# Optimization experiments

Measured on AMD Instinct MI355X. Metric: run time of the kernel, lower is better.

## Reference

```python
import jax, jax.numpy as jnp
import numpy as np
import math

D_MODEL = 1024
N_HEADS = 16
HEAD_DIM = D_MODEL // N_HEADS
B, T = 4, 2048


def setup_inputs() -> dict:
    key = jax.random.key(0)
    k1, k2, k3, k4, k5 = jax.random.split(key, 5)
    s = 1.0 / math.sqrt(D_MODEL)
    return {
        "x": jax.random.normal(k1, (B, T, D_MODEL), dtype=jnp.float32),
        "qkv_w": jax.random.normal(k2, (3 * D_MODEL, D_MODEL), dtype=jnp.float32) * s,
        "qkv_b": jax.random.normal(k3, (3 * D_MODEL,), dtype=jnp.float32) * 0.02,
        "out_w": jax.random.normal(k4, (D_MODEL, D_MODEL), dtype=jnp.float32) * s,
        "out_b": jax.random.normal(k5, (D_MODEL,), dtype=jnp.float32) * 0.02,
    }


def reference(x, qkv_w, qkv_b, out_w, out_b) -> jnp.ndarray:
    b, t, c = x.shape
    h, hd = N_HEADS, HEAD_DIM
    # qkv projection: [B,T,3C]
    qkv = jnp.einsum("btc,oc->bto", x, qkv_w) + qkv_b
    qkv = qkv.reshape(b, t, 3, h, hd).transpose(2, 0, 3, 1, 4)  # [3,B,H,T,hd]
    q, k, v = qkv[0], qkv[1], qkv[2]
    scale = 1.0 / math.sqrt(hd)
    attn = jnp.einsum("bhqd,bhkd->bhqk", q, k) * scale  # [B,H,T,T]
    causal = jnp.triu(jnp.ones((t, t), dtype=bool), k=1)
    attn = jnp.where(causal, -jnp.inf, attn)
    attn = jax.nn.softmax(attn, axis=-1)
    out = jnp.einsum("bhqk,bhkd->bhqd", attn, v)  # [B,H,T,hd]
    out = out.transpose(0, 2, 1, 3).reshape(b, t, c)
    return jnp.einsum("btc,oc->bto", out, out_w) + out_b
```

## Files before the change

kernel.cpp:

```cpp
#include <hip/hip_runtime.h>
#include <stdint.h>
#include <stddef.h>

#define TT 2048
#define NH 16
#define HD 64
#define CM 1024
#define QSCALE 0.1803368801f
#define PPAD 72

typedef float f32x4  __attribute__((ext_vector_type(4)));
typedef short bf16x8 __attribute__((ext_vector_type(8)));

static __device__ __forceinline__ unsigned short f32_to_bf16(float f) {
    union { float f; unsigned u; } c; c.f = f;
    unsigned u = c.u;
    u += 0x7FFFu + ((u >> 16) & 1u);
    return (unsigned short)(u >> 16);
}

static __device__ __forceinline__ unsigned pack_bf16_trunc(float lo, float hi) {
    return __builtin_amdgcn_perm(__float_as_uint(hi), __float_as_uint(lo), 0x07060302u);
}

static __device__ __forceinline__ void glds16(const unsigned short* g, unsigned short* l) {
    __builtin_amdgcn_global_load_lds(
        (const __attribute__((address_space(1))) unsigned int*)g,
        (__attribute__((address_space(3))) unsigned int*)l,
        16, 0, 0);
}

static __device__ __forceinline__ void hard_barrier() {
    asm volatile("s_waitcnt vmcnt(0) lgkmcnt(0)" ::: "memory");
    __syncthreads();
}

__global__ __launch_bounds__(256) void cast_all(
    const float* __restrict__ x, const float* __restrict__ w1,
    const float* __restrict__ w2,
    unsigned short* __restrict__ X16, unsigned short* __restrict__ W1o,
    unsigned short* __restrict__ W2o) {
    int i = blockIdx.x * blockDim.x + threadIdx.x;
    const float* src; unsigned short* dst; int j;
    if (i < 2097152)      { src = x;  dst = X16; j = i; }
    else if (i < 2883584) { src = w1; dst = W1o; j = i - 2097152; }
    else                  { src = w2; dst = W2o; j = i - 2883584; }
    float4 v = ((const float4*)src)[j];
    ushort4 o;
    o.x = f32_to_bf16(v.x); o.y = f32_to_bf16(v.y);
    o.z = f32_to_bf16(v.z); o.w = f32_to_bf16(v.w);
    ((ushort4*)dst)[j] = o;
}

template<bool SWAP>
__device__ __forceinline__ void gemm256_core(
    const unsigned short* __restrict__ A,
    const unsigned short* __restrict__ Bm,
    int m0, int n0,
    unsigned short* lds,
    f32x4 acc[8][4])
{
    const int tid  = threadIdx.x;
    const int lane = tid & 63;
    const int w    = tid >> 6;
    const int l15  = lane & 15;
    const int quad = lane >> 4;
    const int wm   = (w >> 1) * 128;
    const int wn   = (w & 1) * 64;
    const int ro   = (quad ^ (l15 & 3)) * 8;

    const int rr = tid >> 2;
    const int ch = (tid & 3) ^ (rr & 3);
    const unsigned short* gA = A  + (size_t)(m0 + rr) * CM + ch * 8;
    const unsigned short* gB = Bm + (size_t)(n0 + rr) * CM + ch * 8;
    const int wb = (tid & ~63) * 8;

    unsigned short* ldsA = lds;
    unsigned short* ldsB = lds + 16384;

#define STAGE6(bb)                                                    \
    {                                                                 \
        unsigned short* dA = ldsA + (bb) * 8192 + wb;                 \
        unsigned short* dB = ldsB + (bb) * 4096 + wb;                 \
        glds16(gA,            dA);                                    \
        glds16(gA +  64 * CM, dA + 2048);                             \
        glds16(gA + 128 * CM, dA + 4096);                             \
        glds16(gA + 192 * CM, dA + 6144);                             \
        glds16(gB,            dB);                                    \
        glds16(gB +  64 * CM, dB + 2048);                             \
        gA += 32; gB += 32;                                           \
    }

    STAGE6(0);
    STAGE6(1);

    for (int t = 0; t < 32; ++t) {
        if (t > 0) {
            asm volatile("s_waitcnt lgkmcnt(0)" ::: "memory");
            __builtin_amdgcn_s_barrier();
            asm volatile("" ::: "memory");
            if (t + 1 < 32) STAGE6((t + 1) & 1);
        }
        if (t + 1 < 32) asm volatile("s_waitcnt vmcnt(6)" ::: "memory");
        else            asm volatile("s_waitcnt vmcnt(0)" ::: "memory");
        __builtin_amdgcn_s_barrier();
        asm volatile("" ::: "memory");

        const unsigned short* tA = ldsA + (t & 1) * 8192;
        const unsigned short* tB = ldsB + (t & 1) * 4096;

        bf16x8 bfr[4];
        #pragma unroll
        for (int ni = 0; ni < 4; ++ni)
            bfr[ni] = *(const bf16x8*)(tB + (wn + ni * 16 + l15) * 32 + ro);
        bf16x8 af[8];
        #pragma unroll
        for (int mi = 0; mi < 8; ++mi)
            af[mi] = *(const bf16x8*)(tA + (wm + mi * 16 + l15) * 32 + ro);

        #pragma unroll
        for (int mi = 0; mi < 8; ++mi)
            #pragma unroll
            for (int ni = 0; ni < 4; ++ni)
                acc[mi][ni] = SWAP
                    ? __builtin_amdgcn_mfma_f32_16x16x32_bf16(bfr[ni], af[mi], acc[mi][ni], 0, 0, 0)
                    : __builtin_amdgcn_mfma_f32_16x16x32_bf16(af[mi], bfr[ni], acc[mi][ni], 0, 0, 0);
    }
#undef STAGE6
}

__global__ __launch_bounds__(256, 2) void gemm_qkv(
    const unsigned short* __restrict__ X,
    const unsigned short* __restrict__ W,
    const float* __restrict__ bias,
    unsigned short* __restrict__ Qb,
    unsigned short* __restrict__ Kb,
    unsigned short* __restrict__ Vt)
{
    __shared__ __align__(16) unsigned short lds[24576];
    const int m0 = blockIdx.y * 256;
    const int n0 = blockIdx.x * 128;

    f32x4 acc[8][4];
    f32x4 z = {0.f, 0.f, 0.f, 0.f};
    #pragma unroll
    for (int mi = 0; mi < 8; ++mi)
        #pragma unroll
        for (int ni = 0; ni < 4; ++ni) acc[mi][ni] = z;

    const int region = n0 >> 10;
    if (region < 2) gemm256_core<true >(X, W, m0, n0, lds, acc);
    else            gemm256_core<false>(X, W, m0, n0, lds, acc);

    const int tid  = threadIdx.x;
    const int lane = tid & 63;
    const int w    = tid >> 6;
    const int wm   = (w >> 1) * 128;
    const int wn   = (w & 1) * 64;
    const int l15  = lane & 15;
    const int quad = lane >> 4;
    const int b_idx = m0 >> 11;
    const int t0 = m0 & 2047;

    if (region == 2) {
        hard_barrier();
        #pragma unroll
        for (int hn = 0; hn < 2; ++hn) {
            if ((w & 1) == hn) {
                #pragma unroll
                for (int ni = 0; ni < 4; ++ni) {
                    const int nloc = ni * 16 + l15;
                    const float bv = bias[n0 + hn * 64 + nloc];
                    #pragma unroll
                    for (int mi = 0; mi < 8; ++mi) {
                        uint2 pk;
                        pk.x = (unsigned)f32_to_bf16(acc[mi][ni][0] + bv) |
                               ((unsigned)f32_to_bf16(acc[mi][ni][1] + bv) << 16);
                        pk.y = (unsigned)f32_to_bf16(acc[mi][ni][2] + bv) |
                               ((unsigned)f32_to_bf16(acc[mi][ni][3] + bv) << 16);
                        *(uint2*)(lds + nloc * 264 + wm + mi * 16 + quad * 4) = pk;
                    }
                }
            }
            hard_barrier();
            {
                const int row = tid >> 2, seg = tid & 3;
                const int o   = n0 + hn * 64 + row;
                const int oin = o & 1023;
                const int hh  = oin >> 6, d = oin & 63;
                unsigned short* dst = Vt + ((size_t)((b_idx << 4) + hh) * HD + d) * TT
                                        + t0 + seg * 64;
                const unsigned short* src = lds + row * 264 + seg * 64;
                #pragma unroll
                for (int u = 0; u < 8; ++u)
                    *(uint4*)(dst + u * 8) = *(const uint4*)(src + u * 8);
            }
            hard_barrier();
        }
        return;
    }

    unsigned short* dst0 = region ? Kb : Qb;
    const float scl = region ? 1.0f : QSCALE;
    #pragma unroll
    for (int mi = 0; mi < 8; ++mi) {
        const int gm = m0 + wm + mi * 16 + l15;
        const int t  = gm & 2047;
        #pragma unroll
        for (int ni = 0; ni < 4; ++ni) {
            const int o  = n0 + wn + ni * 16 + quad * 4;
            const float4 bv = *(const float4*)(bias + o);
            const int oin = o & 1023;
            const int hh = oin >> 6, d = oin & 63;
            const int bh = (b_idx << 4) + hh;
            const float v0 = (acc[mi][ni][0] + bv.x) * scl;
            const float v1 = (acc[mi][ni][1] + bv.y) * scl;
            const float v2 = (acc[mi][ni][2] + bv.z) * scl;
            const float v3 = (acc[mi][ni][3] + bv.w) * scl;
            uint2 pk;
            pk.x = (unsigned)f32_to_bf16(v0) | ((unsigned)f32_to_bf16(v1) << 16);
            pk.y = (unsigned)f32_to_bf16(v2) | ((unsigned)f32_to_bf16(v3) << 16);
            *(uint2*)(dst0 + (((size_t)(bh * TT + t)) << 6) + d) = pk;
        }
    }
}

__global__ __launch_bounds__(256, 2) void attn_kernel(
    const unsigned short* __restrict__ Qb,
    const unsigned short* __restrict__ Kb,
    const unsigned short* __restrict__ Vt,
    unsigned short* __restrict__ CTX)
{
    __shared__ __align__(16) unsigned short Kl[2][64 * 64];
    __shared__ __align__(16) unsigned short Vl[2][64 * 64];
    __shared__ __align__(16) unsigned short Pl[8][16 * PPAD];

    const int id = blockIdx.x;
    const int qt = 15 - (id >> 6);
    const int bh = id & 63;
    const int b  = bh >> 4, h = bh & 15;
    const int tid  = threadIdx.x;
    const int lane = tid & 63;
    const int w    = tid >> 6;
    const int l15  = lane & 15;
    const int quad = lane >> 4;
    const int sw   = l15 & 7;
    const int bhh  = b * NH + h;

    const unsigned short* Kbase = Kb + (size_t)bhh * TT * HD;
    const unsigned short* Vbase = Vt + (size_t)bhh * HD * TT;
    const f32x4 z = {0.f, 0.f, 0.f, 0.f};

    const int c1 = tid, c2 = tid + 256;
    const int row1 = c1 >> 3, col1 = ((c1 & 7) ^ (row1 & 7)) * 8;
    const int row2 = c2 >> 3, col2 = ((c2 & 7) ^ (row2 & 7)) * 8;
    unsigned short* dK1 = &Kl[0][(c1 & ~63) * 8];
    unsigned short* dK2 = &Kl[0][(c2 & ~63) * 8];
    unsigned short* dV1 = &Vl[0][(c1 & ~63) * 8];
    unsigned short* dV2 = &Vl[0][(c2 & ~63) * 8];

    const int kt_last = 2 * qt + 1;
    const int qb0 = qt * 128;

    const unsigned short* kp1 = Kbase + (size_t)row1 * HD + col1;
    const unsigned short* kp2 = Kbase + (size_t)row2 * HD + col2;
    const unsigned short* vp1 = Vbase + (size_t)row1 * TT + col1;
    const unsigned short* vp2 = Vbase + (size_t)row2 * TT + col2;

    bf16x8 qf[2][2];
    #pragma unroll
    for (int f = 0; f < 2; ++f) {
        const unsigned short* qr =
            Qb + (size_t)(bhh * TT + qb0 + f * 64 + w * 16 + l15) * HD + quad * 8;
        qf[f][0] = *(const bf16x8*)(qr);
        qf[f][1] = *(const bf16x8*)(qr + 32);
    }

    f32x4 o_acc[2][4];
    #pragma unroll
    for (int f = 0; f < 2; ++f)
        #pragma unroll
        for (int di = 0; di < 4; ++di) o_acc[f][di] = z;
    float lrun[2] = {0.f, 0.f};

    glds16(kp1, dK1); glds16(kp2, dK2);
    glds16(vp1, dV1); glds16(vp2, dV2);
    kp1 += 64 * HD; kp2 += 64 * HD; vp1 += 64; vp2 += 64;

    for (int kt = 0; kt <= kt_last; ++kt) {
        const int cur = kt & 1;
        hard_barrier();
        if (kt < kt_last) {
            const int nx = (cur ^ 1) * 4096;
            glds16(kp1, dK1 + nx); glds16(kp2, dK2 + nx);
            glds16(vp1, dV1 + nx); glds16(vp2, dV2 + nx);
            kp1 += 64 * HD; kp2 += 64 * HD; vp1 += 64; vp2 += 64;
        }

        const unsigned short* Kt = Kl[cur];
        const unsigned short* Vtile = Vl[cur];
        const bool f0act = (kt < kt_last);

        f32x4 s0[4], s1[4];
        #pragma unroll
        for (int ni = 0; ni < 4; ++ni) {
            const unsigned short* kr = Kt + (ni * 16 + l15) * 64;
            bf16x8 kf0 = *(const bf16x8*)(kr + ((quad ^ sw) * 8));
            bf16x8 kf1 = *(const bf16x8*)(kr + (((quad + 4) ^ sw) * 8));
            if (f0act) {
                f32x4 a = __builtin_amdgcn_mfma_f32_16x16x32_bf16(kf0, qf[0][0], z, 0, 0, 0);
                s0[ni] = __builtin_amdgcn_mfma_f32_16x16x32_bf16(kf1, qf[0][1], a, 0, 0, 0);
            }
            f32x4 a1 = __builtin_amdgcn_mfma_f32_16x16x32_bf16(kf0, qf[1][0], z, 0, 0, 0);
            s1[ni] = __builtin_amdgcn_mfma_f32_16x16x32_bf16(kf1, qf[1][1], a1, 0, 0, 0);
        }

        const int qloc = w * 16 + l15;
        if (f0act && kt == 2 * qt) {
            #pragma unroll
            for (int ni = 0; ni < 4; ++ni)
                #pragma unroll
                for (int r = 0; r < 4; ++r)
                    if (ni * 16 + quad * 4 + r > qloc) s0[ni][r] = -1e30f;
        }
        if (kt == kt_last) {
            #pragma unroll
            for (int ni = 0; ni < 4; ++ni)
                #pragma unroll
                for (int r = 0; r < 4; ++r)
                    if (ni * 16 + quad * 4 + r > qloc) s1[ni][r] = -1e30f;
        }

        #define SOFTMAX_P(S, F)                                              \
        {                                                                    \
            float acc_l = 0.f;                                               \
            _Pragma("unroll")                                                \
            for (int ni = 0; ni < 4; ++ni)                                   \
                _Pragma("unroll")                                            \
                for (int r = 0; r < 4; ++r) {                                \
                    float p = __builtin_amdgcn_exp2f(S[ni][r]);              \
                    S[ni][r] = p;                                            \
                    acc_l += p;                                              \
                }                                                            \
            lrun[F] += acc_l;                                                \
            unsigned short* pwf = Pl[w * 2 + F];                             \
            _Pragma("unroll")                                                \
            for (int ni = 0; ni < 4; ++ni) {                                 \
                uint2 pk;                                                    \
                pk.x = pack_bf16_trunc(S[ni][0], S[ni][1]);                  \
                pk.y = pack_bf16_trunc(S[ni][2], S[ni][3]);                  \
                *(uint2*)(pwf + l15 * PPAD + ni * 16 + quad * 4) = pk;       \
            }                                                                \
        }

        if (f0act) SOFTMAX_P(s0, 0);
        SOFTMAX_P(s1, 1);
        #undef SOFTMAX_P

        asm volatile("s_waitcnt lgkmcnt(0)" ::: "memory");

        const unsigned short* pw0 = Pl[w * 2 + 0];
        const unsigned short* pw1 = Pl[w * 2 + 1];
        if (f0act) {
            #pragma unroll
            for (int c = 0; c < 2; ++c) {
                bf16x8 pf0 = *(const bf16x8*)(pw0 + l15 * PPAD + c * 32 + quad * 8);
                bf16x8 pf1 = *(const bf16x8*)(pw1 + l15 * PPAD + c * 32 + quad * 8);
                #pragma unroll
                for (int di = 0; di < 4; ++di) {
                    const unsigned short* vr = Vtile + (di * 16 + l15) * 64
                                             + (((c * 4 + quad) ^ sw) * 8);
                    bf16x8 vf = *(const bf16x8*)(vr);
                    o_acc[0][di] = __builtin_amdgcn_mfma_f32_16x16x32_bf16(vf, pf0, o_acc[0][di], 0, 0, 0);
                    o_acc[1][di] = __builtin_amdgcn_mfma_f32_16x16x32_bf16(vf, pf1, o_acc[1][di], 0, 0, 0);
                }
            }
        } else {
            #pragma unroll
            for (int c = 0; c < 2; ++c) {
                bf16x8 pf1 = *(const bf16x8*)(pw1 + l15 * PPAD + c * 32 + quad * 8);
                #pragma unroll
                for (int di = 0; di < 4; ++di) {
                    const unsigned short* vr = Vtile + (di * 16 + l15) * 64
                                             + (((c * 4 + quad) ^ sw) * 8);
                    bf16x8 vf = *(const bf16x8*)(vr);
                    o_acc[1][di] = __builtin_amdgcn_mfma_f32_16x16x32_bf16(vf, pf1, o_acc[1][di], 0, 0, 0);
                }
            }
        }
    }

    #pragma unroll
    for (int f = 0; f < 2; ++f) {
        float lt = lrun[f];
        lt += __shfl_xor(lt, 16);
        lt += __shfl_xor(lt, 32);
        const float inv = 1.0f / lt;
        unsigned short* crow =
            CTX + (size_t)(b * TT + qb0 + f * 64 + w * 16 + l15) * CM + h * HD;
        #pragma unroll
        for (int di = 0; di < 4; ++di) {
            uint2 pk;
            pk.x = (unsigned)f32_to_bf16(o_acc[f][di][0] * inv) |
                   ((unsigned)f32_to_bf16(o_acc[f][di][1] * inv) << 16);
            pk.y = (unsigned)f32_to_bf16(o_acc[f][di][2] * inv) |
                   ((unsigned)f32_to_bf16(o_acc[f][di][3] * inv) << 16);
            *(uint2*)(crow + di * 16 + quad * 4) = pk;
        }
    }
}

__global__ __launch_bounds__(256, 2) void gemm_out(
    const unsigned short* __restrict__ CTX,
    const unsigned short* __restrict__ W,
    const float* __restrict__ bias,
    float* __restrict__ out)
{
    __shared__ __align__(16) unsigned short lds[24576];
    const int m0 = blockIdx.y * 256;
    const int n0 = blockIdx.x * 128;

    f32x4 acc[8][4];
    f32x4 z = {0.f, 0.f, 0.f, 0.f};
    #pragma unroll
    for (int mi = 0; mi < 8; ++mi)
        #pragma unroll
        for (int ni = 0; ni < 4; ++ni) acc[mi][ni] = z;

    gemm256_core<true>(CTX, W, m0, n0, lds, acc);

    const int tid  = threadIdx.x;
    const int lane = tid & 63;
    const int w    = tid >> 6;
    const int wm   = (w >> 1) * 128;
    const int wn   = (w & 1) * 64;
    const int l15  = lane & 15;
    const int quad = lane >> 4;

    #pragma unroll
    for (int mi = 0; mi < 8; ++mi) {
        const int gm = m0 + wm + mi * 16 + l15;
        float* orow = out + (size_t)gm * CM;
        #pragma unroll
        for (int ni = 0; ni < 4; ++ni) {
            const int o = n0 + wn + ni * 16 + quad * 4;
            const float4 bv = *(const float4*)(bias + o);
            float4 v;
            v.x = acc[mi][ni][0] + bv.x;
            v.y = acc[mi][ni][1] + bv.y;
            v.z = acc[mi][ni][2] + bv.z;
            v.w = acc[mi][ni][3] + bv.w;
            *(float4*)(orow + o) = v;
        }
    }
}

extern "C" void kernel_launch(void* const* d_in, const int* in_sizes, int n_in,
                              void* d_out, int out_size, void* d_ws, size_t ws_size,
                              hipStream_t stream) {
    const float* x     = (const float*)d_in[0];
    const float* qkv_w = (const float*)d_in[1];
    const float* qkv_b = (const float*)d_in[2];
    const float* out_w = (const float*)d_in[3];
    const float* out_b = (const float*)d_in[4];
    float* out = (float*)d_out;

    char* ws = (char*)d_ws;
    unsigned short* X16 = (unsigned short*)(ws + 0);
    unsigned short* W1  = (unsigned short*)(ws + 16777216);
    unsigned short* W2  = (unsigned short*)(ws + 23068672);
    unsigned short* Qb  = (unsigned short*)(ws + 25165824);
    unsigned short* Kb  = (unsigned short*)(ws + 41943040);
    unsigned short* Vt  = (unsigned short*)(ws + 58720256);
    unsigned short* CTX = (unsigned short*)(ws + 75497472);

    cast_all<<<12288, 256, 0, stream>>>(x, qkv_w, out_w, X16, W1, W2);

    gemm_qkv<<<dim3(24, 32), 256, 0, stream>>>(X16, W1, qkv_b, Qb, Kb, Vt);
    attn_kernel<<<1024, 256, 0, stream>>>(Qb, Kb, Vt, CTX);
    gemm_out<<<dim3(8, 32), 256, 0, stream>>>(CTX, W2, out_b, out);
}
```

Measured before the change: 256.1 us.

## Split long causal attention query tiles into two KV chunks with combine kernel

Query tiles 8-15 now have their key range split into two halves, each handled by its own block. The blocks write unnormalized bf16 partial outputs and row sums into reused workspace, and a new combine kernel merges them. Shorter tiles are interleaved so that no block does more than 16 key tiles, which balances per-block work across 1536 blocks. The cost is an extra kernel launch, extra partial-output traffic, and an extra bf16 rounding of the partials. The softmax row-sum reduction is also reassociated into a tree.

Result: slower. 271.1 us (+5.9%).

```diff
diff --git a/kernel.cpp b/kernel.cpp
--- a/kernel.cpp
+++ b/kernel.cpp
@@ -17,6 +17,10 @@
     unsigned u = c.u;
     u += 0x7FFFu + ((u >> 16) & 1u);
     return (unsigned short)(u >> 16);
+}
+
+static __device__ __forceinline__ float bf16_to_f32(unsigned short h) {
+    union { unsigned u; float f; } c; c.u = ((unsigned)h) << 16; return c.f;
 }
 
 static __device__ __forceinline__ unsigned pack_bf16_trunc(float lo, float hi) {
@@ -229,15 +233,27 @@
     const unsigned short* __restrict__ Qb,
     const unsigned short* __restrict__ Kb,
     const unsigned short* __restrict__ Vt,
-    unsigned short* __restrict__ CTX)
+    unsigned short* __restrict__ CTX,
+    unsigned short* __restrict__ PO,
+    float* __restrict__ PL)
 {
     __shared__ __align__(16) unsigned short Kl[2][64 * 64];
     __shared__ __align__(16) unsigned short Vl[2][64 * 64];
     __shared__ __align__(16) unsigned short Pl[8][16 * PPAD];
 
+    static const signed char E_QT[24]  = {15,15,14,13,12,11,10,9,8,7,14,6,13,5,12,4,11,3,10,2,9,1,8,0};
+    static const signed char E_C0[24]  = {0,16,0,0,0,0,0,0,0,0,16,0,16,0,16,0,16,0,16,0,16,0,16,0};
+    static const signed char E_LEN[24] = {16,16,16,16,16,16,16,16,16,16,14,14,12,12,10,10,8,8,6,6,4,4,2,2};
+    static const signed char E_SL[24]  = {14,15,12,10,8,6,4,2,0,-1,13,-1,11,-1,9,-1,7,-1,5,-1,3,-1,1,-1};
+
     const int id = blockIdx.x;
-    const int qt = 15 - (id >> 6);
+    const int e  = id >> 6;
     const int bh = id & 63;
+    const int qt   = E_QT[e];
+    const int c0   = E_C0[e];
+    const int len  = E_LEN[e];
+    const int slot = E_SL[e];
+
     const int b  = bh >> 4, h = bh & 15;
     const int tid  = threadIdx.x;
     const int lane = tid & 63;
@@ -259,13 +275,12 @@
     unsigned short* dV1 = &Vl[0][(c1 & ~63) * 8];
     unsigned short* dV2 = &Vl[0][(c2 & ~63) * 8];
 
-    const int kt_last = 2 * qt + 1;
     const int qb0 = qt * 128;
 
-    const unsigned short* kp1 = Kbase + (size_t)row1 * HD + col1;
-    const unsigned short* kp2 = Kbase + (size_t)row2 * HD + col2;
-    const unsigned short* vp1 = Vbase + (size_t)row1 * TT + col1;
-    const unsigned short* vp2 = Vbase + (size_t)row2 * TT + col2;
+    const unsigned short* kp1 = Kbase + (size_t)(c0 * 64 + row1) * HD + col1;
+    const unsigned short* kp2 = Kbase + (size_t)(c0 * 64 + row2) * HD + col2;
+    const unsigned short* vp1 = Vbase + (size_t)row1 * TT + c0 * 64 + col1;
+    const unsigned short* vp2 = Vbase + (size_t)row2 * TT + c0 * 64 + col2;
 
     bf16x8 qf[2][2];
     #pragma unroll
@@ -287,10 +302,11 @@
     glds16(vp1, dV1); glds16(vp2, dV2);
     kp1 += 64 * HD; kp2 += 64 * HD; vp1 += 64; vp2 += 64;
 
-    for (int kt = 0; kt <= kt_last; ++kt) {
-        const int cur = kt & 1;
+    for (int i = 0; i < len; ++i) {
+        const int kt  = c0 + i;
+        const int cur = i & 1;
         hard_barrier();
-        if (kt < kt_last) {
+        if (i + 1 < len) {
             const int nx = (cur ^ 1) * 4096;
             glds16(kp1, dK1 + nx); glds16(kp2, dK2 + nx);
             glds16(vp1, dV1 + nx); glds16(vp2, dV2 + nx);
@@ -299,7 +315,7 @@
 
         const unsigned short* Kt = Kl[cur];
         const unsigned short* Vtile = Vl[cur];
-        const bool f0act = (kt < kt_last);
+        const bool f0act = (kt < 2 * qt + 1);
 
         f32x4 s0[4], s1[4];
         #pragma unroll
@@ -323,7 +339,7 @@
                 for (int r = 0; r < 4; ++r)
                     if (ni * 16 + quad * 4 + r > qloc) s0[ni][r] = -1e30f;
         }
-        if (kt == kt_last) {
+        if (kt == 2 * qt + 1) {
             #pragma unroll
             for (int ni = 0; ni < 4; ++ni)
                 #pragma unroll
@@ -333,16 +349,17 @@
 
         #define SOFTMAX_P(S, F)                                              \
         {                                                                    \
-            float acc_l = 0.f;                                               \
+            float tni[4];                                                    \
             _Pragma("unroll")                                                \
-            for (int ni = 0; ni < 4; ++ni)                                   \
-                _Pragma("unroll")                                            \
-                for (int r = 0; r < 4; ++r) {                                \
-                    float p = __builtin_amdgcn_exp2f(S[ni][r]);              \
-                    S[ni][r] = p;                                            \
-                    acc_l += p;                                              \
-                }                                                            \
-            lrun[F] += acc_l;                                                \
+            for (int ni = 0; ni < 4; ++ni) {                                 \
+                float p0 = __builtin_amdgcn_exp2f(S[ni][0]);                 \
+                float p1 = __builtin_amdgcn_exp2f(S[ni][1]);                 \
+                float p2 = __builtin_amdgcn_exp2f(S[ni][2]);                 \
+                float p3 = __builtin_amdgcn_exp2f(S[ni][3]);                 \
+                S[ni][0] = p0; S[ni][1] = p1; S[ni][2] = p2; S[ni][3] = p3;  \
+                tni[ni] = (p0 + p1) + (p2 + p3);                             \
+            }                                                                \
+            lrun[F] += (tni[0] + tni[1]) + (tni[2] + tni[3]);                \
             unsigned short* pwf = Pl[w * 2 + F];                             \
             _Pragma("unroll")                                                \
             for (int ni = 0; ni < 4; ++ni) {                                 \
@@ -390,23 +407,86 @@
         }
     }
 
-    #pragma unroll
-    for (int f = 0; f < 2; ++f) {
-        float lt = lrun[f];
-        lt += __shfl_xor(lt, 16);
-        lt += __shfl_xor(lt, 32);
-        const float inv = 1.0f / lt;
-        unsigned short* crow =
-            CTX + (size_t)(b * TT + qb0 + f * 64 + w * 16 + l15) * CM + h * HD;
-        #pragma unroll
-        for (int di = 0; di < 4; ++di) {
-            uint2 pk;
-            pk.x = (unsigned)f32_to_bf16(o_acc[f][di][0] * inv) |
-                   ((unsigned)f32_to_bf16(o_acc[f][di][1] * inv) << 16);
-            pk.y = (unsigned)f32_to_bf16(o_acc[f][di][2] * inv) |
-                   ((unsigned)f32_to_bf16(o_acc[f][di][3] * inv) << 16);
-            *(uint2*)(crow + di * 16 + quad * 4) = pk;
-        }
+    if (slot < 0) {
+        #pragma unroll
+        for (int f = 0; f < 2; ++f) {
+            float lt = lrun[f];
+            lt += __shfl_xor(lt, 16);
+            lt += __shfl_xor(lt, 32);
+            const float inv = 1.0f / lt;
+            unsigned short* crow =
+                CTX + (size_t)(b * TT + qb0 + f * 64 + w * 16 + l15) * CM + h * HD;
+            #pragma unroll
+            for (int di = 0; di < 4; ++di) {
+                uint2 pk;
+                pk.x = (unsigned)f32_to_bf16(o_acc[f][di][0] * inv) |
+                       ((unsigned)f32_to_bf16(o_acc[f][di][1] * inv) << 16);
+                pk.y = (unsigned)f32_to_bf16(o_acc[f][di][2] * inv) |
+                       ((unsigned)f32_to_bf16(o_acc[f][di][3] * inv) << 16);
+                *(uint2*)(crow + di * 16 + quad * 4) = pk;
+            }
+        }
+    } else {
+        const size_t pb = ((size_t)slot * 64 + bh) * 8192;
+        const size_t lb = ((size_t)slot * 64 + bh) * 128;
+        #pragma unroll
+        for (int f = 0; f < 2; ++f) {
+            float lt = lrun[f];
+            lt += __shfl_xor(lt, 16);
+            lt += __shfl_xor(lt, 32);
+            const int row = f * 64 + w * 16 + l15;
+            if (quad == 0) PL[lb + row] = lt;
+            unsigned short* prow = PO + pb + (size_t)row * 64;
+            #pragma unroll
+            for (int di = 0; di < 4; ++di) {
+                uint2 pk;
+                pk.x = (unsigned)f32_to_bf16(o_acc[f][di][0]) |
+                       ((unsigned)f32_to_bf16(o_acc[f][di][1]) << 16);
+                pk.y = (unsigned)f32_to_bf16(o_acc[f][di][2]) |
+                       ((unsigned)f32_to_bf16(o_acc[f][di][3]) << 16);
+                *(uint2*)(prow + di * 16 + quad * 4) = pk;
+            }
+        }
+    }
+}
+
+__global__ __launch_bounds__(256) void attn_combine(
+    const unsigned short* __restrict__ PO,
+    const float* __restrict__ PL,
+    unsigned short* __restrict__ CTX)
+{
+    const int id = blockIdx.x;
+    const int qi = id >> 6;
+    const int bh = id & 63;
+    const int b = bh >> 4, h = bh & 15;
+    const size_t bA = ((size_t)(qi * 2 + 0) * 64 + bh) * 8192;
+    const size_t bB = ((size_t)(qi * 2 + 1) * 64 + bh) * 8192;
+    const size_t lA = ((size_t)(qi * 2 + 0) * 64 + bh) * 128;
+    const size_t lB = ((size_t)(qi * 2 + 1) * 64 + bh) * 128;
+    const int t = threadIdx.x;
+    #pragma unroll
+    for (int u = 0; u < 4; ++u) {
+        const int idx = u * 256 + t;
+        const int row = idx >> 3, d0 = (idx & 7) * 8;
+        const bf16x8 a = *(const bf16x8*)(PO + bA + row * 64 + d0);
+        const bf16x8 c = *(const bf16x8*)(PO + bB + row * 64 + d0);
+        const float inv = 1.0f / (PL[lA + row] + PL[lB + row]);
+        uint2 pk0, pk1;
+        float o0 = (bf16_to_f32((unsigned short)a[0]) + bf16_to_f32((unsigned short)c[0])) * inv;
+        float o1 = (bf16_to_f32((unsigned short)a[1]) + bf16_to_f32((unsigned short)c[1])) * inv;
+        float o2 = (bf16_to_f32((unsigned short)a[2]) + bf16_to_f32((unsigned short)c[2])) * inv;
+        float o3 = (bf16_to_f32((unsigned short)a[3]) + bf16_to_f32((unsigned short)c[3])) * inv;
+        float o4 = (bf16_to_f32((unsigned short)a[4]) + bf16_to_f32((unsigned short)c[4])) * inv;
+        float o5 = (bf16_to_f32((unsigned short)a[5]) + bf16_to_f32((unsigned short)c[5])) * inv;
+        float o6 = (bf16_to_f32((unsigned short)a[6]) + bf16_to_f32((unsigned short)c[6])) * inv;
+        float o7 = (bf16_to_f32((unsigned short)a[7]) + bf16_to_f32((unsigned short)c[7])) * inv;
+        pk0.x = (unsigned)f32_to_bf16(o0) | ((unsigned)f32_to_bf16(o1) << 16);
+        pk0.y = (unsigned)f32_to_bf16(o2) | ((unsigned)f32_to_bf16(o3) << 16);
+        pk1.x = (unsigned)f32_to_bf16(o4) | ((unsigned)f32_to_bf16(o5) << 16);
+        pk1.y = (unsigned)f32_to_bf16(o6) | ((unsigned)f32_to_bf16(o7) << 16);
+        unsigned short* dst = CTX + ((size_t)(b * TT + (8 + qi) * 128 + row)) * CM + h * HD + d0;
+        uint4 pk; pk.x = pk0.x; pk.y = pk0.y; pk.z = pk1.x; pk.w = pk1.y;
+        *(uint4*)dst = pk;
     }
 }
 
@@ -474,9 +554,13 @@
     unsigned short* Vt  = (unsigned short*)(ws + 58720256);
     unsigned short* CTX = (unsigned short*)(ws + 75497472);
 
+    unsigned short* PO = X16;
+    float*          PL = (float*)W1;
+
     cast_all<<<12288, 256, 0, stream>>>(x, qkv_w, out_w, X16, W1, W2);
 
     gemm_qkv<<<dim3(24, 32), 256, 0, stream>>>(X16, W1, qkv_b, Qb, Kb, Vt);
-    attn_kernel<<<1024, 256, 0, stream>>>(Qb, Kb, Vt, CTX);
+    attn_kernel<<<1536, 256, 0, stream>>>(Qb, Kb, Vt, CTX, PO, PL);
+    attn_combine<<<512, 256, 0, stream>>>(PO, PL, CTX);
     gemm_out<<<dim3(8, 32), 256, 0, stream>>>(CTX, W2, out_b, out);
 }
```

## Triple-buffer K/V tiles with explicit vmcnt waits and share one P buffer

Applied to the files above, without the earlier changes.

Moves the attention inner loop from double to triple buffering of K/V tiles in LDS, issuing loads two tiles ahead and using vmcnt-based waits plus barriers instead of a hard barrier. The P scratch buffer is cut from two per wave to one, so the s1 and s0 softmax/PV phases run one after the other, with V fragments cached in registers for reuse. This aims to hide global load latency and keep LDS usage roughly flat. The cost is extra barriers, higher register pressure from the held V fragments, and serialized P writes.

Result: slower. 262.0 us (+2.3%).

```diff
diff --git a/kernel.cpp b/kernel.cpp
--- a/kernel.cpp
+++ b/kernel.cpp
@@ -231,9 +231,9 @@
     const unsigned short* __restrict__ Vt,
     unsigned short* __restrict__ CTX)
 {
-    __shared__ __align__(16) unsigned short Kl[2][64 * 64];
-    __shared__ __align__(16) unsigned short Vl[2][64 * 64];
-    __shared__ __align__(16) unsigned short Pl[8][16 * PPAD];
+    __shared__ __align__(16) unsigned short Kl[3][4096];
+    __shared__ __align__(16) unsigned short Vl[3][4096];
+    __shared__ __align__(16) unsigned short Pl[4][16 * PPAD];
 
     const int id = blockIdx.x;
     const int qt = 15 - (id >> 6);
@@ -259,7 +259,7 @@
     unsigned short* dV1 = &Vl[0][(c1 & ~63) * 8];
     unsigned short* dV2 = &Vl[0][(c2 & ~63) * 8];
 
-    const int kt_last = 2 * qt + 1;
+    const int len = 2 * qt + 2;
     const int qb0 = qt * 128;
 
     const unsigned short* kp1 = Kbase + (size_t)row1 * HD + col1;
@@ -283,23 +283,34 @@
         for (int di = 0; di < 4; ++di) o_acc[f][di] = z;
     float lrun[2] = {0.f, 0.f};
 
-    glds16(kp1, dK1); glds16(kp2, dK2);
-    glds16(vp1, dV1); glds16(vp2, dV2);
-    kp1 += 64 * HD; kp2 += 64 * HD; vp1 += 64; vp2 += 64;
-
-    for (int kt = 0; kt <= kt_last; ++kt) {
-        const int cur = kt & 1;
-        hard_barrier();
-        if (kt < kt_last) {
-            const int nx = (cur ^ 1) * 4096;
-            glds16(kp1, dK1 + nx); glds16(kp2, dK2 + nx);
-            glds16(vp1, dV1 + nx); glds16(vp2, dV2 + nx);
-            kp1 += 64 * HD; kp2 += 64 * HD; vp1 += 64; vp2 += 64;
-        }
-
-        const unsigned short* Kt = Kl[cur];
-        const unsigned short* Vtile = Vl[cur];
-        const bool f0act = (kt < kt_last);
+#define STAGE_KV(bufidx)                                               \
+    {                                                                  \
+        const int nx = (bufidx) * 4096;                                \
+        glds16(kp1, dK1 + nx); glds16(kp2, dK2 + nx);                  \
+        glds16(vp1, dV1 + nx); glds16(vp2, dV2 + nx);                  \
+        kp1 += 64 * HD; kp2 += 64 * HD; vp1 += 64; vp2 += 64;          \
+    }
+    STAGE_KV(0);
+    STAGE_KV(1);
+    if (len > 2) STAGE_KV(2);
+
+    for (int i = 0; i < len; ++i) {
+        const int cur = i % 3;
+        if (i > 0) {
+            asm volatile("s_waitcnt lgkmcnt(0)" ::: "memory");
+            __builtin_amdgcn_s_barrier();
+            asm volatile("" ::: "memory");
+            if (i + 2 < len) STAGE_KV((i + 2) % 3);
+        }
+        if (i + 2 < len)      asm volatile("s_waitcnt vmcnt(8)" ::: "memory");
+        else if (i + 1 < len) asm volatile("s_waitcnt vmcnt(4)" ::: "memory");
+        else                  asm volatile("s_waitcnt vmcnt(0)" ::: "memory");
+        __builtin_amdgcn_s_barrier();
+        asm volatile("" ::: "memory");
+
+        const unsigned short* Kt    = &Kl[0][0] + cur * 4096;
+        const unsigned short* Vtile = &Vl[0][0] + cur * 4096;
+        const bool f0act = (i < len - 1);
 
         f32x4 s0[4], s1[4];
         #pragma unroll
@@ -316,14 +327,14 @@
         }
 
         const int qloc = w * 16 + l15;
-        if (f0act && kt == 2 * qt) {
+        if (f0act && i == len - 2) {
             #pragma unroll
             for (int ni = 0; ni < 4; ++ni)
                 #pragma unroll
                 for (int r = 0; r < 4; ++r)
                     if (ni * 16 + quad * 4 + r > qloc) s0[ni][r] = -1e30f;
         }
-        if (kt == kt_last) {
+        if (i == len - 1) {
             #pragma unroll
             for (int ni = 0; ni < 4; ++ni)
                 #pragma unroll
@@ -333,17 +344,18 @@
 
         #define SOFTMAX_P(S, F)                                              \
         {                                                                    \
-            float acc_l = 0.f;                                               \
+            float tni[4];                                                    \
             _Pragma("unroll")                                                \
-            for (int ni = 0; ni < 4; ++ni)                                   \
-                _Pragma("unroll")                                            \
-                for (int r = 0; r < 4; ++r) {                                \
-                    float p = __builtin_amdgcn_exp2f(S[ni][r]);              \
-                    S[ni][r] = p;                                            \
-                    acc_l += p;                                              \
-                }                                                            \
-            lrun[F] += acc_l;                                                \
-            unsigned short* pwf = Pl[w * 2 + F];                             \
+            for (int ni = 0; ni < 4; ++ni) {                                 \
+                float p0 = __builtin_amdgcn_exp2f(S[ni][0]);                 \
+                float p1 = __builtin_amdgcn_exp2f(S[ni][1]);                 \
+                float p2 = __builtin_amdgcn_exp2f(S[ni][2]);                 \
+                float p3 = __builtin_amdgcn_exp2f(S[ni][3]);                 \
+                S[ni][0] = p0; S[ni][1] = p1; S[ni][2] = p2; S[ni][3] = p3;  \
+                tni[ni] = (p0 + p1) + (p2 + p3);                             \
+            }                                                                \
+            lrun[F] += (tni[0] + tni[1]) + (tni[2] + tni[3]);                \
+            unsigned short* pwf = Pl[w];                                     \
             _Pragma("unroll")                                                \
             for (int ni = 0; ni < 4; ++ni) {                                 \
                 uint2 pk;                                                    \
@@ -353,42 +365,33 @@
             }                                                                \
         }
 
-        if (f0act) SOFTMAX_P(s0, 0);
+        bf16x8 vf[2][4];
         SOFTMAX_P(s1, 1);
-        #undef SOFTMAX_P
-
         asm volatile("s_waitcnt lgkmcnt(0)" ::: "memory");
-
-        const unsigned short* pw0 = Pl[w * 2 + 0];
-        const unsigned short* pw1 = Pl[w * 2 + 1];
+        #pragma unroll
+        for (int c = 0; c < 2; ++c) {
+            bf16x8 pf1 = *(const bf16x8*)(Pl[w] + l15 * PPAD + c * 32 + quad * 8);
+            #pragma unroll
+            for (int di = 0; di < 4; ++di) {
+                vf[c][di] = *(const bf16x8*)(Vtile + (di * 16 + l15) * 64
+                                           + (((c * 4 + quad) ^ sw) * 8));
+                o_acc[1][di] = __builtin_amdgcn_mfma_f32_16x16x32_bf16(vf[c][di], pf1, o_acc[1][di], 0, 0, 0);
+            }
+        }
         if (f0act) {
+            SOFTMAX_P(s0, 0);
+            asm volatile("s_waitcnt lgkmcnt(0)" ::: "memory");
             #pragma unroll
             for (int c = 0; c < 2; ++c) {
-                bf16x8 pf0 = *(const bf16x8*)(pw0 + l15 * PPAD + c * 32 + quad * 8);
-                bf16x8 pf1 = *(const bf16x8*)(pw1 + l15 * PPAD + c * 32 + quad * 8);
+                bf16x8 pf0 = *(const bf16x8*)(Pl[w] + l15 * PPAD + c * 32 + quad * 8);
                 #pragma unroll
-                for (int di = 0; di < 4; ++di) {
-                    const unsigned short* vr = Vtile + (di * 16 + l15) * 64
-                                             + (((c * 4 + quad) ^ sw) * 8);
-                    bf16x8 vf = *(const bf16x8*)(vr);
-                    o_acc[0][di] = __builtin_amdgcn_mfma_f32_16x16x32_bf16(vf, pf0, o_acc[0][di], 0, 0, 0);
-                    o_acc[1][di] = __builtin_amdgcn_mfma_f32_16x16x32_bf16(vf, pf1, o_acc[1][di], 0, 0, 0);
-                }
+                for (int di = 0; di < 4; ++di)
+                    o_acc[0][di] = __builtin_amdgcn_mfma_f32_16x16x32_bf16(vf[c][di], pf0, o_acc[0][di], 0, 0, 0);
             }
-        } else {
-            #pragma unroll
-            for (int c = 0; c < 2; ++c) {
-                bf16x8 pf1 = *(const bf16x8*)(pw1 + l15 * PPAD + c * 32 + quad * 8);
-                #pragma unroll
-                for (int di = 0; di < 4; ++di) {
-                    const unsigned short* vr = Vtile + (di * 16 + l15) * 64
-                                             + (((c * 4 + quad) ^ sw) * 8);
-                    bf16x8 vf = *(const bf16x8*)(vr);
-                    o_acc[1][di] = __builtin_amdgcn_mfma_f32_16x16x32_bf16(vf, pf1, o_acc[1][di], 0, 0, 0);
-                }
-            }
-        }
-    }
+        }
+        #undef SOFTMAX_P
+    }
+#undef STAGE_KV
 
     #pragma unroll
     for (int f = 0; f < 2; ++f) {
```
